# Performance work log

Measured on AMD Instinct MI355X. Metric: run time of the kernel, lower is better.

Reference implementation:

```python
import jax, jax.numpy as jnp
import numpy as np

H = 16  # num_heads

def setup_inputs() -> dict:
    key = jax.random.key(0)
    k1, k2, k3 = jax.random.split(key, 3)
    D = 1024
    x = jax.random.normal(k1, (4, 2048, D), dtype=jnp.float32)
    W_qkv = jax.random.normal(k2, (D, 3 * D), dtype=jnp.float32) * (1.0 / np.sqrt(D))
    b_qkv = jnp.zeros((3 * D,), dtype=jnp.float32)
    W_out = jax.random.normal(k3, (D, D), dtype=jnp.float32) * (1.0 / np.sqrt(D))
    b_out = jnp.zeros((D,), dtype=jnp.float32)
    return {"x": x, "W_qkv": W_qkv, "b_qkv": b_qkv, "W_out": W_out, "b_out": b_out}

def reference(x, W_qkv, b_qkv, W_out, b_out):
    B, S, D = x.shape
    hd = D // H  # head_dim
    qkv = x @ W_qkv + b_qkv  # [B,S,3D]
    q, k, v = jnp.split(qkv, 3, axis=-1)
    # [B,S,D] -> [B,H,S,hd]
    q = q.reshape(B, S, H, hd).transpose(0, 2, 1, 3)
    k = k.reshape(B, S, H, hd).transpose(0, 2, 1, 3)
    v = v.reshape(B, S, H, hd).transpose(0, 2, 1, 3)
    scores = jnp.einsum('bhqd,bhkd->bhqk', q, k) / jnp.sqrt(jnp.float32(hd))
    weights = jax.nn.softmax(scores, axis=-1)  # dropout p=0.0 (eval)
    out = jnp.einsum('bhqk,bhkd->bhqd', weights, v)
    out = out.transpose(0, 2, 1, 3).reshape(B, S, D)
    return out @ W_out + b_out
```

## Files before the change

### kernel.cpp

```cpp
#include <hip/hip_runtime.h>

typedef __bf16 bf16;
typedef __bf16 bf16x8 __attribute__((ext_vector_type(8)));
typedef __bf16 bf16x4 __attribute__((ext_vector_type(4)));
typedef short s16x4 __attribute__((ext_vector_type(4)));
typedef float f32x4 __attribute__((ext_vector_type(4)));

static constexpr int NB = 4;
static constexpr int NS = 2048;
static constexpr int ND = 1024;
static constexpr int NH = 16;
static constexpr int HD = 64;
static constexpr float QSCALE = 0.18033688011112042f;

#define GL16(g, l)                                                             \
    __builtin_amdgcn_global_load_lds(                                          \
        (const __attribute__((address_space(1))) void*)(g),                    \
        (__attribute__((address_space(3))) void*)(l), 16, 0, 0)

static __device__ __forceinline__ unsigned pk2(float a, float b) {
    union { __bf16 h[2]; unsigned u; } t;
    t.h[0] = (__bf16)a; t.h[1] = (__bf16)b;
    return t.u;
}

__global__ void k_conv(const float* __restrict__ in, bf16* __restrict__ out, int n) {
    int i = (blockIdx.x * blockDim.x + threadIdx.x) * 4;
    if (i < n) {
        float4 v = *reinterpret_cast<const float4*>(in + i);
        bf16* o = out + i;
        o[0] = (bf16)v.x; o[1] = (bf16)v.y; o[2] = (bf16)v.z; o[3] = (bf16)v.w;
    }
}

__global__ void k_transconv(const float* __restrict__ in, bf16* __restrict__ out,
                            int K, int N) {
    __shared__ float tile[32][33];
    int k0 = blockIdx.y * 32, n0 = blockIdx.x * 32;
    int tx = threadIdx.x, ty = threadIdx.y;
    for (int j = 0; j < 32; j += 8)
        tile[ty + j][tx] = in[(long)(k0 + ty + j) * N + n0 + tx];
    __syncthreads();
    for (int j = 0; j < 32; j += 8)
        out[(long)(n0 + ty + j) * K + k0 + tx] = (bf16)tile[tx][ty + j];
}

template <int EPI>
__global__ __launch_bounds__(256, 2) void k_gemm(
    const bf16* __restrict__ A, const bf16* __restrict__ Bt,
    const float* __restrict__ bias,
    void* __restrict__ out0, void* __restrict__ out1, void* __restrict__ out2,
    int M, int N, int Kd)
{
    constexpr int BM = 128, BN = 128, BK = 64;
    __shared__ __align__(16) bf16 As[2][BM * BK];
    __shared__ __align__(16) bf16 Bs[2][BN * BK];

    const int t = threadIdx.x;
    const int wid = t >> 6, lane = t & 63;
    const int wm = wid >> 1, wn = wid & 1;
    const int m0 = blockIdx.y * BM, n0 = blockIdx.x * BN;
    const int lrow = lane & 15, lhi = lane >> 4;

    const int srow0 = wid * 32 + (lane >> 3);
    const int scol = ((lane & 7) ^ (lane >> 3)) * 8;
    const bf16* ag = A + (long)(m0 + srow0) * Kd + scol;
    const bf16* bg = Bt + (long)(n0 + srow0) * Kd + scol;

    auto STAGE = [&](int buf_, int k0_) {
#pragma unroll
        for (int c = 0; c < 4; ++c) {
            GL16(ag + (long)(c * 8) * Kd + k0_, &As[buf_][(wid * 32 + c * 8) * BK]);
            GL16(bg + (long)(c * 8) * Kd + k0_, &Bs[buf_][(wid * 32 + c * 8) * BK]);
        }
    };

    f32x4 acc[4][4] = {};
    const int nt = Kd >> 6;
    const int swzr = (lrow & 7) << 4;
    int co[2];
#pragma unroll
    for (int kk = 0; kk < 2; ++kk)
        co[kk] = ((kk * 64 + lhi * 16) ^ swzr) >> 1;

    STAGE(0, 0);
    __syncthreads();
    int cur = 0;
    for (int tix = 0; tix < nt; ++tix) {
        if (tix + 1 < nt) STAGE(cur ^ 1, (tix + 1) * BK);

        bf16x8 af[2][4], bfr[2][4];
#pragma unroll
        for (int kk = 0; kk < 2; ++kk)
#pragma unroll
            for (int i = 0; i < 4; ++i) {
                af[kk][i]  = *reinterpret_cast<const bf16x8*>(
                    &As[cur][(wm * 64 + i * 16 + lrow) * BK + co[kk]]);
                bfr[kk][i] = *reinterpret_cast<const bf16x8*>(
                    &Bs[cur][(wn * 64 + i * 16 + lrow) * BK + co[kk]]);
            }
        __builtin_amdgcn_s_setprio(1);
#pragma unroll
        for (int kk = 0; kk < 2; ++kk)
#pragma unroll
            for (int i = 0; i < 4; ++i)
#pragma unroll
                for (int j = 0; j < 4; ++j)
                    acc[i][j] = __builtin_amdgcn_mfma_f32_16x16x32_bf16(
                        af[kk][i], bfr[kk][j], acc[i][j], 0, 0, 0);
        __builtin_amdgcn_s_setprio(0);
        __syncthreads();
        cur ^= 1;
    }

    if (EPI == 0) {
        bf16* Qb = (bf16*)out0; bf16* Kb = (bf16*)out1; bf16* Vt = (bf16*)out2;
#pragma unroll
        for (int j = 0; j < 4; ++j) {
            int col = n0 + wn * 64 + j * 16 + lrow;
            float bv = bias[col];
            int which = col >> 10;
            int rem = col & 1023;
            int h = rem >> 6, d = rem & 63;
#pragma unroll
            for (int i = 0; i < 4; ++i) {
                int mbase = m0 + wm * 64 + i * 16 + lhi * 4;
#pragma unroll
                for (int r = 0; r < 4; ++r) {
                    int row = mbase + r;
                    int bb = row >> 11, s = row & 2047;
                    long bh = bb * NH + h;
                    float v = acc[i][j][r] + bv;
                    if (which == 0)      Qb[(bh * NS + s) * HD + d] = (bf16)(v * QSCALE);
                    else if (which == 1) Kb[(bh * NS + s) * HD + d] = (bf16)v;
                    else                 Vt[(bh * HD + d) * NS + s] = (bf16)v;
                }
            }
        }
    } else {
        float* O = (float*)out0;
#pragma unroll
        for (int j = 0; j < 4; ++j) {
            int col = n0 + wn * 64 + j * 16 + lrow;
            float bv = bias[col];
#pragma unroll
            for (int i = 0; i < 4; ++i) {
                int mbase = m0 + wm * 64 + i * 16 + lhi * 4;
#pragma unroll
                for (int r = 0; r < 4; ++r)
                    O[(long)(mbase + r) * N + col] = acc[i][j][r] + bv;
            }
        }
    }
}

__global__ __launch_bounds__(256, 4) void k_attn(
    const bf16* __restrict__ Qb, const bf16* __restrict__ Kb,
    const bf16* __restrict__ Vt, bf16* __restrict__ Ao)
{
    constexpr int KB = 64;
    constexpr int NT = NS / KB;
    __shared__ __align__(16) bf16 Ks[2][KB * HD];
    __shared__ __align__(16) bf16 Vs[2][HD * KB];

    const int t = threadIdx.x;
    const int wid = t >> 6, lane = t & 63;
    const int lrow = lane & 15, lhi = lane >> 4;

    const int flat = blockIdx.y * gridDim.x + blockIdx.x;
    const int n = (flat & 7) * 128 + (flat >> 3);
    const int bh = n >> 4;
    const int qblk = (n & 15) * 128;
    const int qw = qblk + wid * 32;

    const bf16* Qg = Qb + ((long)bh * NS + qw) * HD;
    const bf16* Kg = Kb + (long)bh * NS * HD;
    const bf16* Vg = Vt + (long)bh * HD * NS;

    bf16x8 qf[2][2];
#pragma unroll
    for (int qfr = 0; qfr < 2; ++qfr)
#pragma unroll
        for (int c = 0; c < 2; ++c)
            qf[qfr][c] = *reinterpret_cast<const bf16x8*>(
                Qg + (long)(qfr * 16 + lrow) * HD + c * 32 + lhi * 8);

    f32x4 of[2][4] = {};
    float lsum[2] = {0.f, 0.f};

    const int gsr = lane >> 3;
    const int gsc = ((lane & 7) ^ gsr) * 8;
    auto STAGE = [&](int buf, int kb) {
#pragma unroll
        for (int c = 0; c < 2; ++c) {
            const int rb = wid * 16 + c * 8;
            GL16(Kg + (long)(kb + rb + gsr) * HD + gsc, &Ks[buf][rb * 64]);
            GL16(Vg + (long)(rb + gsr) * NS + kb + gsc, &Vs[buf][rb * 64]);
        }
    };

    const int rsw = (lrow & 7) << 4;

#define COMPUTE(b_, i_)                                                        \
    {                                                                          \
        f32x4 st[2][4] = {};                                                   \
        __builtin_amdgcn_s_setprio(1);                                         \
        _Pragma("unroll")                                                      \
        for (int j = 0; j < 4; ++j) {                                          \
            _Pragma("unroll")                                                  \
            for (int c = 0; c < 2; ++c) {                                      \
                bf16x8 kf = *reinterpret_cast<const bf16x8*>(                  \
                    &Ks[b_][(j * 16 + lrow) * 64 +                             \
                            (((c * 64 + lhi * 16) ^ rsw) >> 1)]);              \
                _Pragma("unroll")                                              \
                for (int qfr = 0; qfr < 2; ++qfr)                              \
                    st[qfr][j] = __builtin_amdgcn_mfma_f32_16x16x32_bf16(      \
                        kf, qf[qfr][c], st[qfr][j], 0, 0, 0);                  \
            }                                                                  \
        }                                                                      \
        __builtin_amdgcn_s_setprio(0);                                         \
        union { unsigned u[2]; s16x4 s; } pf[2][4];                            \
        _Pragma("unroll")                                                      \
        for (int qfr = 0; qfr < 2; ++qfr)                                      \
            _Pragma("unroll")                                                  \
            for (int j = 0; j < 4; ++j) {                                      \
                float e0 = __builtin_amdgcn_exp2f(st[qfr][j][0]);              \
                float e1 = __builtin_amdgcn_exp2f(st[qfr][j][1]);              \
                float e2 = __builtin_amdgcn_exp2f(st[qfr][j][2]);              \
                float e3 = __builtin_amdgcn_exp2f(st[qfr][j][3]);              \
                lsum[qfr] += (e0 + e1) + (e2 + e3);                            \
                pf[qfr][j].u[0] = pk2(e0, e1);                                 \
                pf[qfr][j].u[1] = pk2(e2, e3);                                 \
            }                                                                  \
        __builtin_amdgcn_s_setprio(1);                                         \
        _Pragma("unroll")                                                      \
        for (int j = 0; j < 4; ++j) {                                          \
            _Pragma("unroll")                                                  \
            for (int f = 0; f < 4; ++f) {                                      \
                s16x4 vf = *reinterpret_cast<const s16x4*>(                    \
                    &Vs[b_][(f * 16 + lrow) * 64 +                             \
                            (((j * 32 + lhi * 8) ^ rsw) >> 1)]);               \
                _Pragma("unroll")                                              \
                for (int qfr = 0; qfr < 2; ++qfr)                              \
                    of[qfr][f] = __builtin_amdgcn_mfma_f32_16x16x16bf16_1k(    \
                        vf, pf[qfr][j].s, of[qfr][f], 0, 0, 0);                \
            }                                                                  \
        }                                                                      \
        __builtin_amdgcn_s_setprio(0);                                         \
    }

    STAGE(0, 0);
    for (int it = 0; it < NT; it += 2) {
        __syncthreads();
        STAGE(1, (it + 1) * KB);
        COMPUTE(0, it);
        __syncthreads();
        if (it + 2 < NT) STAGE(0, (it + 2) * KB);
        COMPUTE(1, it + 1);
    }
#undef COMPUTE

#pragma unroll
    for (int qfr = 0; qfr < 2; ++qfr) {
        lsum[qfr] += __shfl_xor(lsum[qfr], 16);
        lsum[qfr] += __shfl_xor(lsum[qfr], 32);
    }

    const int bb = bh >> 4, h = bh & 15;
#pragma unroll
    for (int qfr = 0; qfr < 2; ++qfr) {
        float inv = 1.0f / lsum[qfr];
        int s = qw + qfr * 16 + lrow;
#pragma unroll
        for (int f = 0; f < 4; ++f) {
            bf16x4 o4;
#pragma unroll
            for (int r = 0; r < 4; ++r) o4[r] = (bf16)(of[qfr][f][r] * inv);
            *reinterpret_cast<bf16x4*>(
                &Ao[((long)bb * NS + s) * ND + h * HD + f * 16 + 4 * lhi]) = o4;
        }
    }
}

extern "C" void kernel_launch(void* const* d_in, const int* in_sizes, int n_in,
                              void* d_out, int out_size, void* d_ws, size_t ws_size,
                              hipStream_t stream) {
    const float* x    = (const float*)d_in[0];
    const float* Wqkv = (const float*)d_in[1];
    const float* bqkv = (const float*)d_in[2];
    const float* Wout = (const float*)d_in[3];
    const float* bout = (const float*)d_in[4];
    float* out = (float*)d_out;

    char* ws = (char*)d_ws;
    bf16* Xb  = (bf16*)(ws);
    bf16* Wqt = (bf16*)(ws + 16777216);
    bf16* Wot = (bf16*)(ws + 23068672);
    bf16* Qb  = (bf16*)(ws + 25165824);
    bf16* Kb  = (bf16*)(ws + 41943040);
    bf16* Vt  = (bf16*)(ws + 58720256);
    bf16* Ab  = (bf16*)(ws + 75497472);

    k_conv<<<dim3(8192), dim3(256), 0, stream>>>(x, Xb, NB * NS * ND);
    k_transconv<<<dim3(96, 32), dim3(32, 8), 0, stream>>>(Wqkv, Wqt, ND, 3 * ND);
    k_transconv<<<dim3(32, 32), dim3(32, 8), 0, stream>>>(Wout, Wot, ND, ND);

    k_gemm<0><<<dim3(24, 64), dim3(256), 0, stream>>>(
        Xb, Wqt, bqkv, Qb, Kb, Vt, NB * NS, 3 * ND, ND);

    k_attn<<<dim3(16, 64), dim3(256), 0, stream>>>(Qb, Kb, Vt, Ab);

    k_gemm<1><<<dim3(8, 64), dim3(256), 0, stream>>>(
        Ab, Wot, bout, out, nullptr, nullptr, NB * NS, ND, ND);
}
```

Measured before the change: 233.2 us.

## Route P through LDS to use 16x16x32 MFMA for PV product

The attention kernel now writes the exponentiated score tile P to a per-wave LDS buffer and reads it back in the transposed layout. This lets the PV product use the wider 16x16x32 bf16 MFMA with P as the A operand, replacing twice as many 16x16x16 MFMAs, and the output store is re-indexed to match the transposed accumulator layout. The cost is extra LDS writes and reads per tile (8KB more shared memory, which may affect occupancy), plus scalar bf16 output stores and shuffles for the row sums.

After: 221.5 us. 1.05x faster.

```diff
diff --git a/kernel.cpp b/kernel.cpp
--- a/kernel.cpp
+++ b/kernel.cpp
@@ -2,9 +2,8 @@
 
 typedef __bf16 bf16;
 typedef __bf16 bf16x8 __attribute__((ext_vector_type(8)));
-typedef __bf16 bf16x4 __attribute__((ext_vector_type(4)));
-typedef short s16x4 __attribute__((ext_vector_type(4)));
 typedef float f32x4 __attribute__((ext_vector_type(4)));
+typedef unsigned u32x2 __attribute__((ext_vector_type(2)));
 
 static constexpr int NB = 4;
 static constexpr int NS = 2048;
@@ -162,6 +161,7 @@
     constexpr int NT = NS / KB;
     __shared__ __align__(16) bf16 Ks[2][KB * HD];
     __shared__ __align__(16) bf16 Vs[2][HD * KB];
+    __shared__ __align__(16) bf16 Ps[4 * 16 * 64];
 
     const int t = threadIdx.x;
     const int wid = t >> 6, lane = t & 63;
@@ -170,8 +170,7 @@
     const int flat = blockIdx.y * gridDim.x + blockIdx.x;
     const int n = (flat & 7) * 128 + (flat >> 3);
     const int bh = n >> 4;
-    const int qblk = (n & 15) * 128;
-    const int qw = qblk + wid * 32;
+    const int qw = (n & 15) * 128 + wid * 32;
 
     const bf16* Qg = Qb + ((long)bh * NS + qw) * HD;
     const bf16* Kg = Kb + (long)bh * NS * HD;
@@ -200,65 +199,66 @@
     };
 
     const int rsw = (lrow & 7) << 4;
-
-#define COMPUTE(b_, i_)                                                        \
-    {                                                                          \
-        f32x4 st[2][4] = {};                                                   \
-        __builtin_amdgcn_s_setprio(1);                                         \
-        _Pragma("unroll")                                                      \
-        for (int j = 0; j < 4; ++j) {                                          \
-            _Pragma("unroll")                                                  \
-            for (int c = 0; c < 2; ++c) {                                      \
-                bf16x8 kf = *reinterpret_cast<const bf16x8*>(                  \
-                    &Ks[b_][(j * 16 + lrow) * 64 +                             \
-                            (((c * 64 + lhi * 16) ^ rsw) >> 1)]);              \
-                _Pragma("unroll")                                              \
-                for (int qfr = 0; qfr < 2; ++qfr)                              \
-                    st[qfr][j] = __builtin_amdgcn_mfma_f32_16x16x32_bf16(      \
-                        kf, qf[qfr][c], st[qfr][j], 0, 0, 0);                  \
-            }                                                                  \
-        }                                                                      \
-        __builtin_amdgcn_s_setprio(0);                                         \
-        union { unsigned u[2]; s16x4 s; } pf[2][4];                            \
-        _Pragma("unroll")                                                      \
-        for (int qfr = 0; qfr < 2; ++qfr)                                      \
-            _Pragma("unroll")                                                  \
-            for (int j = 0; j < 4; ++j) {                                      \
-                float e0 = __builtin_amdgcn_exp2f(st[qfr][j][0]);              \
-                float e1 = __builtin_amdgcn_exp2f(st[qfr][j][1]);              \
-                float e2 = __builtin_amdgcn_exp2f(st[qfr][j][2]);              \
-                float e3 = __builtin_amdgcn_exp2f(st[qfr][j][3]);              \
-                lsum[qfr] += (e0 + e1) + (e2 + e3);                            \
-                pf[qfr][j].u[0] = pk2(e0, e1);                                 \
-                pf[qfr][j].u[1] = pk2(e2, e3);                                 \
-            }                                                                  \
-        __builtin_amdgcn_s_setprio(1);                                         \
-        _Pragma("unroll")                                                      \
-        for (int j = 0; j < 4; ++j) {                                          \
-            _Pragma("unroll")                                                  \
-            for (int f = 0; f < 4; ++f) {                                      \
-                s16x4 vf = *reinterpret_cast<const s16x4*>(                    \
-                    &Vs[b_][(f * 16 + lrow) * 64 +                             \
-                            (((j * 32 + lhi * 8) ^ rsw) >> 1)]);               \
-                _Pragma("unroll")                                              \
-                for (int qfr = 0; qfr < 2; ++qfr)                              \
-                    of[qfr][f] = __builtin_amdgcn_mfma_f32_16x16x16bf16_1k(    \
-                        vf, pf[qfr][j].s, of[qfr][f], 0, 0, 0);                \
-            }                                                                  \
-        }                                                                      \
-        __builtin_amdgcn_s_setprio(0);                                         \
-    }
+    bf16* psw = &Ps[wid * 1024 + lrow * 64];
+
+    auto COMPUTE = [&](int b_) {
+        f32x4 st[2][4] = {};
+        __builtin_amdgcn_s_setprio(1);
+#pragma unroll
+        for (int j = 0; j < 4; ++j)
+#pragma unroll
+            for (int c = 0; c < 2; ++c) {
+                bf16x8 kf = *reinterpret_cast<const bf16x8*>(
+                    &Ks[b_][(j * 16 + lrow) * 64 + (((c * 64 + lhi * 16) ^ rsw) >> 1)]);
+#pragma unroll
+                for (int qfr = 0; qfr < 2; ++qfr)
+                    st[qfr][j] = __builtin_amdgcn_mfma_f32_16x16x32_bf16(
+                        kf, qf[qfr][c], st[qfr][j], 0, 0, 0);
+            }
+        __builtin_amdgcn_s_setprio(0);
+
+#pragma unroll
+        for (int qfr = 0; qfr < 2; ++qfr) {
+#pragma unroll
+            for (int j = 0; j < 4; ++j) {
+                float e0 = __builtin_amdgcn_exp2f(st[qfr][j][0]);
+                float e1 = __builtin_amdgcn_exp2f(st[qfr][j][1]);
+                float e2 = __builtin_amdgcn_exp2f(st[qfr][j][2]);
+                float e3 = __builtin_amdgcn_exp2f(st[qfr][j][3]);
+                lsum[qfr] += (e0 + e1) + (e2 + e3);
+                u32x2 w; w[0] = pk2(e0, e1); w[1] = pk2(e2, e3);
+                *reinterpret_cast<u32x2*>(
+                    reinterpret_cast<char*>(psw) + (((j * 32 + lhi * 8) ^ rsw))) = w;
+            }
+            asm volatile("" ::: "memory");
+#pragma unroll
+            for (int chunk = 0; chunk < 2; ++chunk) {
+                bf16x8 pf = *reinterpret_cast<const bf16x8*>(
+                    reinterpret_cast<char*>(psw) + ((chunk * 64 + lhi * 16) ^ rsw));
+                __builtin_amdgcn_s_setprio(1);
+#pragma unroll
+                for (int f = 0; f < 4; ++f) {
+                    bf16x8 vf = *reinterpret_cast<const bf16x8*>(
+                        &Vs[b_][(f * 16 + lrow) * 64 +
+                                (((chunk * 64 + lhi * 16) ^ rsw) >> 1)]);
+                    of[qfr][f] = __builtin_amdgcn_mfma_f32_16x16x32_bf16(
+                        pf, vf, of[qfr][f], 0, 0, 0);
+                }
+                __builtin_amdgcn_s_setprio(0);
+            }
+            asm volatile("" ::: "memory");
+        }
+    };
 
     STAGE(0, 0);
     for (int it = 0; it < NT; it += 2) {
         __syncthreads();
         STAGE(1, (it + 1) * KB);
-        COMPUTE(0, it);
+        COMPUTE(0);
         __syncthreads();
         if (it + 2 < NT) STAGE(0, (it + 2) * KB);
-        COMPUTE(1, it + 1);
-    }
-#undef COMPUTE
+        COMPUTE(1);
+    }
 
 #pragma unroll
     for (int qfr = 0; qfr < 2; ++qfr) {
@@ -269,15 +269,14 @@
     const int bb = bh >> 4, h = bh & 15;
 #pragma unroll
     for (int qfr = 0; qfr < 2; ++qfr) {
-        float inv = 1.0f / lsum[qfr];
-        int s = qw + qfr * 16 + lrow;
-#pragma unroll
-        for (int f = 0; f < 4; ++f) {
-            bf16x4 o4;
-#pragma unroll
-            for (int r = 0; r < 4; ++r) o4[r] = (bf16)(of[qfr][f][r] * inv);
-            *reinterpret_cast<bf16x4*>(
-                &Ao[((long)bb * NS + s) * ND + h * HD + f * 16 + 4 * lhi]) = o4;
+#pragma unroll
+        for (int r = 0; r < 4; ++r) {
+            float inv = 1.0f / __shfl(lsum[qfr], 4 * lhi + r);
+            int s = qw + qfr * 16 + 4 * lhi + r;
+#pragma unroll
+            for (int f = 0; f < 4; ++f)
+                Ao[((long)bb * NS + s) * ND + h * HD + f * 16 + lrow] =
+                    (bf16)(of[qfr][f][r] * inv);
         }
     }
 }
```
